# Optimization experiments

Measured on AMD Instinct MI355X. Metric: run time of the kernel, lower is better.

Reference implementation:

```python
import jax, jax.numpy as jnp
import numpy as np

N = 50000
DEG = 16
E = N * DEG
IN_F, HID, OUT_F = 512, 128, 64
SLOPE = 0.2


def setup_inputs() -> dict:
    key = jax.random.key(0)
    ks = jax.random.split(key, 10)
    row_ptr = jnp.arange(N + 1, dtype=jnp.int64) * DEG          # uniform-degree CSR
    col_idx = jax.random.randint(ks[0], (E,), 0, N, dtype=jnp.int64)
    x = jax.random.normal(ks[1], (N, IN_F), dtype=jnp.float32)
    s1 = 1.0 / np.sqrt(IN_F)
    s2 = 1.0 / np.sqrt(HID)
    return {
        "row_ptr": row_ptr,
        "col_idx": col_idx,
        "input_feature": x,
        "W1": jax.random.normal(ks[2], (IN_F, HID), dtype=jnp.float32) * s1,
        "attn_l1": jax.random.normal(ks[3], (HID,), dtype=jnp.float32) * s2,
        "attn_r1": jax.random.normal(ks[4], (HID,), dtype=jnp.float32) * s2,
        "bias1": jnp.zeros((HID,), dtype=jnp.float32),
        "W2": jax.random.normal(ks[5], (HID, OUT_F), dtype=jnp.float32) * s2,
        "attn_l2": jax.random.normal(ks[6], (OUT_F,), dtype=jnp.float32) * 0.125,
        "attn_r2": jax.random.normal(ks[7], (OUT_F,), dtype=jnp.float32) * 0.125,
        "bias2": jnp.zeros((OUT_F,), dtype=jnp.float32),
    }


def gat_layer(row_ptr, col_idx, x, W, attn_l, attn_r, bias):
    n = row_ptr.shape[0] - 1
    e = col_idx.shape[0]
    h = x @ W                                   # [N, F] dense GEMM
    el = h @ attn_l                             # [N] dst attention term
    er = h @ attn_r                             # [N] src attention term
    # edge -> destination row via CSR row_ptr
    dst = jnp.searchsorted(row_ptr, jnp.arange(e, dtype=row_ptr.dtype), side="right") - 1
    src = col_idx
    score = jax.nn.leaky_relu(el[dst] + er[src], negative_slope=SLOPE)  # [E]
    # neighborhood softmax over edges sharing a destination
    smax = jax.ops.segment_max(score, dst, num_segments=n)
    ex = jnp.exp(score - smax[dst])
    ssum = jax.ops.segment_sum(ex, dst, num_segments=n)
    alpha = ex / ssum[dst]                      # [E]
    # weighted gather-scatter aggregation
    out = jax.ops.segment_sum(alpha[:, None] * h[src], dst, num_segments=n)
    return out + bias


def reference(row_ptr, col_idx, input_feature, W1, attn_l1, attn_r1, bias1,
              W2, attn_l2, attn_r2, bias2):
    x = gat_layer(row_ptr, col_idx, input_feature, W1, attn_l1, attn_r1, bias1)
    x = gat_layer(row_ptr, col_idx, x, W2, attn_l2, attn_r2, bias2)
    return x
```

## Files before the change

### kernel.cpp

```cpp
#include <hip/hip_runtime.h>
#include <hip/hip_bf16.h>

#define Nn 50000
#define DEG 16
#define IN_F 512
#define HID 128
#define OUT_F 64
#define SLOPE 0.2f

typedef __attribute__((ext_vector_type(8))) short bf16x8;
typedef __attribute__((ext_vector_type(4))) float f32x4;
typedef __attribute__((ext_vector_type(2))) float f32x2;
typedef __attribute__((ext_vector_type(4))) unsigned int u32x4;

__device__ __forceinline__ unsigned short f2bf(float f) {
    return __builtin_bit_cast(unsigned short, __float2bfloat16(f));
}
__device__ __forceinline__ float bf2f(unsigned short u) {
    return __bfloat162float(__builtin_bit_cast(__hip_bfloat16, u));
}
__device__ __forceinline__ void async_copy16(const void* g, void* l) {
    __builtin_amdgcn_global_load_lds(
        (const __attribute__((address_space(1))) unsigned int*)g,
        (__attribute__((address_space(3))) unsigned int*)l, 16, 0, 0);
}

__global__ void __launch_bounds__(256) prep_kernel(
        const float* __restrict__ W1, const float* __restrict__ W2,
        const int* __restrict__ row_ptr,
        unsigned short* __restrict__ w1c, unsigned short* __restrict__ w2t,
        int* __restrict__ flag64) {
    int g = blockIdx.x * 256 + threadIdx.x;
    if (g == 0) {
        *flag64 = (row_ptr[1] == DEG) ? 0 : 1;
    }
    if (g < IN_F * HID) {
        int k = g >> 7, c = g & 127;
        int ch = k >> 7, kl = k & 127;
        int s  = kl >> 3, j = kl & 7;
        int sp = s ^ (c & 7);
        w1c[ch * 16384 + c * 128 + sp * 8 + j] = f2bf(W1[g]);
    } else {
        int g2 = g - IN_F * HID;
        if (g2 < HID * OUT_F) {
            int k = g2 >> 6, c = g2 & 63;
            w2t[c * HID + k] = f2bf(W2[g2]);
        }
    }
}

template<int K>
__global__ void __launch_bounds__(256) gemm1_lds(
        const float* __restrict__ Af, const unsigned short* __restrict__ w1c,
        const float* __restrict__ alv, const float* __restrict__ arv,
        unsigned short* __restrict__ Hb, float* __restrict__ el,
        float* __restrict__ er, int M) {
    constexpr int F   = 128;
    constexpr int NT  = 8;
    constexpr int NCH = K / 128;
    __shared__ unsigned short bt[128 * 128];

    const int tid  = threadIdx.x;
    const int lane = tid & 63;
    const int w    = tid >> 6;
    const int ln   = lane & 15, q = lane >> 4;
    const int mb   = blockIdx.x * 64 + w * 16;

    int m0 = mb + ln; if (m0 > M - 1) m0 = M - 1;
    const float* a0p = Af + (size_t)m0 * K;

    f32x4 acc[NT] = {};

    for (int ch = 0; ch < NCH; ++ch) {
        const char* gch = (const char*)w1c + ch * 32768;
        #pragma unroll
        for (int i = 0; i < 8; ++i) {
            int slot = w * 8 + i;
            async_copy16(gch + slot * 1024 + lane * 16, (char*)bt + slot * 1024);
        }
        __syncthreads();

        f32x4 ap[4][2];
        #pragma unroll
        for (int ks = 0; ks < 4; ++ks) {
            const int kk = ch * 128 + ks * 32 + q * 8;
            ap[ks][0] = *(const f32x4*)(a0p + kk);
            ap[ks][1] = *(const f32x4*)(a0p + kk + 4);
        }
        #pragma unroll
        for (int ks = 0; ks < 4; ++ks) {
            bf16x8 af;
            #pragma unroll
            for (int jj = 0; jj < 4; ++jj) {
                af[jj]     = (short)f2bf(ap[ks][0][jj]);
                af[jj + 4] = (short)f2bf(ap[ks][1][jj]);
            }
            #pragma unroll
            for (int nt = 0; nt < NT; ++nt) {
                const int c  = nt * 16 + ln;
                const int sp = (ks * 4 + q) ^ (ln & 7);
                bf16x8 bfr = *(const bf16x8*)&bt[c * 128 + sp * 8];
                acc[nt] = __builtin_amdgcn_mfma_f32_16x16x32_bf16(af, bfr, acc[nt], 0, 0, 0);
            }
        }
        __syncthreads();
    }

    float av[NT], bv[NT];
    #pragma unroll
    for (int nt = 0; nt < NT; ++nt) {
        av[nt] = alv[nt * 16 + ln];
        bv[nt] = arv[nt * 16 + ln];
    }
    #pragma unroll
    for (int r = 0; r < 4; ++r) {
        float sl = 0.f, sr = 0.f;
        #pragma unroll
        for (int nt = 0; nt < NT; ++nt) {
            float v = acc[nt][r];
            sl += v * av[nt];
            sr += v * bv[nt];
        }
        #pragma unroll
        for (int m = 1; m < 16; m <<= 1) {
            sl += __shfl_xor(sl, m);
            sr += __shfl_xor(sr, m);
        }
        int grow = mb + q * 4 + r;
        if (grow < M) {
            #pragma unroll
            for (int nt = 0; nt < NT; ++nt)
                Hb[(size_t)grow * F + nt * 16 + ln] = f2bf(acc[nt][r]);
            if (ln == 0) { el[grow] = sl; er[grow] = sr; }
        }
    }
}

__global__ void __launch_bounds__(256) fused_agg_gemm2(
        const int* __restrict__ col, const int* __restrict__ flag64,
        const float* __restrict__ el1, const float* __restrict__ er1,
        const unsigned short* __restrict__ Hb, const float* __restrict__ b1,
        const unsigned short* __restrict__ w2t,
        const float* __restrict__ al2, const float* __restrict__ ar2,
        unsigned short* __restrict__ H2, float* __restrict__ el2,
        float* __restrict__ er2) {
    constexpr int STR = 136;
    __shared__ unsigned short at[16 * STR];
    __shared__ float redl[16][4];
    __shared__ float redr[16][4];

    const int tid  = threadIdx.x;
    const int lane = tid & 63;
    const int w    = tid >> 6;
    const int ln   = lane & 15, q = lane >> 4;
    const int nb   = blockIdx.x * 16;
    const int use64 = *flag64;

    {
        int node = nb + w * 4 + q;
        int e    = node * DEG + ln;
        int src  = use64 ? (int)((const long long*)col)[e] : col[e];
        float sc = el1[node] + er1[src];
        sc = sc >= 0.f ? sc : SLOPE * sc;
        float mx = sc;
        #pragma unroll
        for (int m = 1; m < 16; m <<= 1) mx = fmaxf(mx, __shfl_xor(mx, m, 16));
        float ex = __expf(sc - mx);
        float sm = ex;
        #pragma unroll
        for (int m = 1; m < 16; m <<= 1) sm += __shfl_xor(sm, m, 16);
        float alpha = ex / sm;

        float a[8] = {};
        #pragma unroll
        for (int jj = 0; jj < DEG; ++jj) {
            int   sl_ = q * 16 + jj;
            int   sj = __shfl(src, sl_);
            float aj = __shfl(alpha, sl_);
            bf16x8 hv = *(const bf16x8*)&Hb[(size_t)sj * HID + ln * 8];
            #pragma unroll
            for (int c = 0; c < 8; ++c)
                a[c] += aj * bf2f((unsigned short)hv[c]);
        }
        unsigned int pk[4];
        #pragma unroll
        for (int c = 0; c < 4; ++c) {
            float lo = a[2 * c]     + b1[ln * 8 + 2 * c];
            float hi = a[2 * c + 1] + b1[ln * 8 + 2 * c + 1];
            pk[c] = (unsigned int)f2bf(lo) | ((unsigned int)f2bf(hi) << 16);
        }
        *(u32x4*)&at[(w * 4 + q) * STR + ln * 8] = *(u32x4*)pk;
    }
    __syncthreads();

    f32x4 acc = {};
    const unsigned short* bb = w2t + (size_t)(w * 16 + ln) * HID;
    #pragma unroll
    for (int ks = 0; ks < HID / 32; ++ks) {
        bf16x8 af  = *(const bf16x8*)&at[ln * STR + ks * 32 + q * 8];
        bf16x8 bfr = *(const bf16x8*)&bb[ks * 32 + q * 8];
        acc = __builtin_amdgcn_mfma_f32_16x16x32_bf16(af, bfr, acc, 0, 0, 0);
    }

    float av = al2[w * 16 + ln], bv = ar2[w * 16 + ln];
    #pragma unroll
    for (int r = 0; r < 4; ++r) {
        float v  = acc[r];
        float sl = v * av, sr = v * bv;
        #pragma unroll
        for (int m = 1; m < 16; m <<= 1) {
            sl += __shfl_xor(sl, m, 16);
            sr += __shfl_xor(sr, m, 16);
        }
        int rowl = q * 4 + r;
        H2[(size_t)(nb + rowl) * OUT_F + w * 16 + ln] = f2bf(v);
        if (ln == 0) { redl[rowl][w] = sl; redr[rowl][w] = sr; }
    }
    __syncthreads();
    if (tid < 16) {
        el2[nb + tid] = redl[tid][0] + redl[tid][1] + redl[tid][2] + redl[tid][3];
        er2[nb + tid] = redr[tid][0] + redr[tid][1] + redr[tid][2] + redr[tid][3];
    }
}

__global__ void __launch_bounds__(256) agg2_k(
        const int* __restrict__ col, const int* __restrict__ flag64,
        const float* __restrict__ el, const float* __restrict__ er,
        const unsigned short* __restrict__ Hb, const float* __restrict__ bias,
        float* __restrict__ out) {
    int lane = threadIdx.x & 63;
    int node = blockIdx.x * 4 + (threadIdx.x >> 6);
    int j    = lane & 15;
    int e    = node * DEG + j;
    int src  = (*flag64) ? (int)((const long long*)col)[e] : col[e];
    float sc = el[node] + er[src];
    sc = sc >= 0.f ? sc : SLOPE * sc;
    float mx = sc;
    #pragma unroll
    for (int m = 1; m < 16; m <<= 1) mx = fmaxf(mx, __shfl_xor(mx, m, 16));
    float ex = __expf(sc - mx);
    float sm = ex;
    #pragma unroll
    for (int m = 1; m < 16; m <<= 1) sm += __shfl_xor(sm, m, 16);
    float alpha = ex / sm;

    int h = lane >> 5;
    int c = lane & 31;
    float a0 = 0.f, a1 = 0.f;
    #pragma unroll
    for (int jj = 0; jj < DEG; jj += 2) {
        int   sj = __shfl(src, jj + h, 16);
        float aj = __shfl(alpha, jj + h, 16);
        unsigned int hv = *(const unsigned int*)&Hb[(size_t)sj * OUT_F + c * 2];
        a0 += aj * bf2f((unsigned short)(hv & 0xffffu));
        a1 += aj * bf2f((unsigned short)(hv >> 16));
    }
    a0 += __shfl_xor(a0, 32);
    a1 += __shfl_xor(a1, 32);
    if (h == 0) {
        f32x2 o;
        o[0] = a0 + bias[c * 2];
        o[1] = a1 + bias[c * 2 + 1];
        *(f32x2*)&out[(size_t)node * OUT_F + c * 2] = o;
    }
}

extern "C" void kernel_launch(void* const* d_in, const int* in_sizes, int n_in,
                              void* d_out, int out_size, void* d_ws, size_t ws_size,
                              hipStream_t stream) {
    const int*   row_ptr = (const int*)d_in[0];
    const int*   col_idx = (const int*)d_in[1];
    const float* x   = (const float*)d_in[2];
    const float* W1  = (const float*)d_in[3];
    const float* al1 = (const float*)d_in[4];
    const float* ar1 = (const float*)d_in[5];
    const float* b1  = (const float*)d_in[6];
    const float* W2  = (const float*)d_in[7];
    const float* al2 = (const float*)d_in[8];
    const float* ar2 = (const float*)d_in[9];
    const float* b2  = (const float*)d_in[10];
    float* out = (float*)d_out;

    float* ws = (float*)d_ws;
    unsigned short* h1b = (unsigned short*)ws;
    unsigned short* h2b = (unsigned short*)(ws + 3200000);
    float* el1 = ws + 5000000;
    float* er1 = ws + 5050000;
    float* el2 = ws + 5100000;
    float* er2 = ws + 5150000;
    unsigned short* w1c = (unsigned short*)(ws + 5200000);
    unsigned short* w2t = (unsigned short*)(ws + 5232768);
    int* flag64 = (int*)(ws + 5236864);

    prep_kernel<<<(IN_F * HID + HID * OUT_F + 255) / 256, 256, 0, stream>>>(
        W1, W2, row_ptr, w1c, w2t, flag64);

    gemm1_lds<512><<<(Nn + 63) / 64, 256, 0, stream>>>(
        x, w1c, al1, ar1, h1b, el1, er1, Nn);

    fused_agg_gemm2<<<Nn / 16, 256, 0, stream>>>(
        col_idx, flag64, el1, er1, h1b, b1, w2t, al2, ar2, h2b, el2, er2);

    agg2_k<<<Nn / 4, 256, 0, stream>>>(col_idx, flag64, el2, er2, h2b, b2, out);
}
```

Before: 231.9 us.

## Fold W1·W2 into one 512x64 weight and aggregate projected features

Because aggregation is linear, layer-1 aggregation followed by the W2 projection is reordered. The code precomputes W12 = W1·W2, the attention vectors W1·attn_l1 and W1·attn_r1, and bias1·W2 in a prep kernel. The main GEMM now produces a 64-wide G = x·W12 directly, with el1/er1 computed as dot products of x against the folded vectors, and it drops the LDS staging of the weights. Layer-1 aggregation then gathers 64-wide bf16 rows instead of 128-wide ones, and the fused GEMM2 stage disappears. The cost is different rounding from the bf16 folded weights, plus uncached direct global loads of the weights inside the GEMM.

```diff
diff --git a/kernel.cpp b/kernel.cpp
--- a/kernel.cpp
+++ b/kernel.cpp
@@ -10,7 +10,6 @@
 
 typedef __attribute__((ext_vector_type(8))) short bf16x8;
 typedef __attribute__((ext_vector_type(4))) float f32x4;
-typedef __attribute__((ext_vector_type(2))) float f32x2;
 typedef __attribute__((ext_vector_type(4))) unsigned int u32x4;
 
 __device__ __forceinline__ unsigned short f2bf(float f) {
@@ -19,47 +18,51 @@
 __device__ __forceinline__ float bf2f(unsigned short u) {
     return __bfloat162float(__builtin_bit_cast(__hip_bfloat16, u));
 }
-__device__ __forceinline__ void async_copy16(const void* g, void* l) {
-    __builtin_amdgcn_global_load_lds(
-        (const __attribute__((address_space(1))) unsigned int*)g,
-        (__attribute__((address_space(3))) unsigned int*)l, 16, 0, 0);
-}
 
 __global__ void __launch_bounds__(256) prep_kernel(
         const float* __restrict__ W1, const float* __restrict__ W2,
-        const int* __restrict__ row_ptr,
-        unsigned short* __restrict__ w1c, unsigned short* __restrict__ w2t,
-        int* __restrict__ flag64) {
-    int g = blockIdx.x * 256 + threadIdx.x;
-    if (g == 0) {
+        const float* __restrict__ al1, const float* __restrict__ ar1,
+        const float* __restrict__ b1, const int* __restrict__ row_ptr,
+        unsigned short* __restrict__ w12t, float* __restrict__ uv,
+        float* __restrict__ c2v, int* __restrict__ flag64) {
+    const int tid = threadIdx.x;
+    const int lane = tid & 63;
+    const int w = tid >> 6;
+    const int k = blockIdx.x * 4 + w;
+    if (blockIdx.x == 0 && tid == 0) {
         *flag64 = (row_ptr[1] == DEG) ? 0 : 1;
     }
-    if (g < IN_F * HID) {
-        int k = g >> 7, c = g & 127;
-        int ch = k >> 7, kl = k & 127;
-        int s  = kl >> 3, j = kl & 7;
-        int sp = s ^ (c & 7);
-        w1c[ch * 16384 + c * 128 + sp * 8 + j] = f2bf(W1[g]);
-    } else {
-        int g2 = g - IN_F * HID;
-        if (g2 < HID * OUT_F) {
-            int k = g2 >> 6, c = g2 & 63;
-            w2t[c * HID + k] = f2bf(W2[g2]);
-        }
+    const float* w1row = W1 + (size_t)k * HID;
+
+    float acc = 0.f;
+    #pragma unroll 8
+    for (int j = 0; j < HID; ++j)
+        acc += w1row[j] * W2[j * OUT_F + lane];
+    w12t[(size_t)lane * IN_F + k] = f2bf(acc);
+
+    float pu = w1row[lane] * al1[lane] + w1row[lane + 64] * al1[lane + 64];
+    float pv = w1row[lane] * ar1[lane] + w1row[lane + 64] * ar1[lane + 64];
+    #pragma unroll
+    for (int m = 1; m < 64; m <<= 1) {
+        pu += __shfl_xor(pu, m);
+        pv += __shfl_xor(pv, m);
+    }
+    if (lane == 0) { uv[k] = pu; uv[IN_F + k] = pv; }
+
+    if (blockIdx.x == 0 && w == 0) {
+        float cacc = 0.f;
+        #pragma unroll 8
+        for (int j = 0; j < HID; ++j) cacc += b1[j] * W2[j * OUT_F + lane];
+        c2v[lane] = cacc;
     }
 }
 
 template<int K>
-__global__ void __launch_bounds__(256) gemm1_lds(
-        const float* __restrict__ Af, const unsigned short* __restrict__ w1c,
-        const float* __restrict__ alv, const float* __restrict__ arv,
-        unsigned short* __restrict__ Hb, float* __restrict__ el,
+__global__ void __launch_bounds__(256) gemm1_direct(
+        const float* __restrict__ Af, const unsigned short* __restrict__ w12t,
+        const float* __restrict__ uv,
+        unsigned short* __restrict__ G, float* __restrict__ el,
         float* __restrict__ er, int M) {
-    constexpr int F   = 128;
-    constexpr int NT  = 8;
-    constexpr int NCH = K / 128;
-    __shared__ unsigned short bt[128 * 128];
-
     const int tid  = threadIdx.x;
     const int lane = tid & 63;
     const int w    = tid >> 6;
@@ -69,170 +72,65 @@
     int m0 = mb + ln; if (m0 > M - 1) m0 = M - 1;
     const float* a0p = Af + (size_t)m0 * K;
 
-    f32x4 acc[NT] = {};
-
-    for (int ch = 0; ch < NCH; ++ch) {
-        const char* gch = (const char*)w1c + ch * 32768;
-        #pragma unroll
-        for (int i = 0; i < 8; ++i) {
-            int slot = w * 8 + i;
-            async_copy16(gch + slot * 1024 + lane * 16, (char*)bt + slot * 1024);
-        }
-        __syncthreads();
-
-        f32x4 ap[4][2];
-        #pragma unroll
-        for (int ks = 0; ks < 4; ++ks) {
-            const int kk = ch * 128 + ks * 32 + q * 8;
-            ap[ks][0] = *(const f32x4*)(a0p + kk);
-            ap[ks][1] = *(const f32x4*)(a0p + kk + 4);
-        }
-        #pragma unroll
-        for (int ks = 0; ks < 4; ++ks) {
-            bf16x8 af;
-            #pragma unroll
-            for (int jj = 0; jj < 4; ++jj) {
-                af[jj]     = (short)f2bf(ap[ks][0][jj]);
-                af[jj + 4] = (short)f2bf(ap[ks][1][jj]);
-            }
-            #pragma unroll
-            for (int nt = 0; nt < NT; ++nt) {
-                const int c  = nt * 16 + ln;
-                const int sp = (ks * 4 + q) ^ (ln & 7);
-                bf16x8 bfr = *(const bf16x8*)&bt[c * 128 + sp * 8];
-                acc[nt] = __builtin_amdgcn_mfma_f32_16x16x32_bf16(af, bfr, acc[nt], 0, 0, 0);
-            }
-        }
-        __syncthreads();
-    }
-
-    float av[NT], bv[NT];
-    #pragma unroll
-    for (int nt = 0; nt < NT; ++nt) {
-        av[nt] = alv[nt * 16 + ln];
-        bv[nt] = arv[nt * 16 + ln];
-    }
+    f32x4 acc[4] = {};
+    float sl = 0.f, sr = 0.f;
+
+    #pragma unroll 4
+    for (int ks = 0; ks < K / 32; ++ks) {
+        const int kk = ks * 32 + q * 8;
+        f32x4 ap0 = *(const f32x4*)(a0p + kk);
+        f32x4 ap1 = *(const f32x4*)(a0p + kk + 4);
+        f32x4 u0  = *(const f32x4*)(uv + kk);
+        f32x4 u1_ = *(const f32x4*)(uv + kk + 4);
+        f32x4 v0  = *(const f32x4*)(uv + K + kk);
+        f32x4 v1_ = *(const f32x4*)(uv + K + kk + 4);
+        bf16x8 af;
+        #pragma unroll
+        for (int jj = 0; jj < 4; ++jj) {
+            af[jj]     = (short)f2bf(ap0[jj]);
+            af[jj + 4] = (short)f2bf(ap1[jj]);
+            sl += ap0[jj] * u0[jj] + ap1[jj] * u1_[jj];
+            sr += ap0[jj] * v0[jj] + ap1[jj] * v1_[jj];
+        }
+        #pragma unroll
+        for (int nt = 0; nt < 4; ++nt) {
+            bf16x8 bfr = *(const bf16x8*)&w12t[(size_t)(nt * 16 + ln) * K + kk];
+            acc[nt] = __builtin_amdgcn_mfma_f32_16x16x32_bf16(af, bfr, acc[nt], 0, 0, 0);
+        }
+    }
+
+    sl += __shfl_xor(sl, 16); sl += __shfl_xor(sl, 32);
+    sr += __shfl_xor(sr, 16); sr += __shfl_xor(sr, 32);
+    if (q == 0 && mb + ln < M) { el[mb + ln] = sl; er[mb + ln] = sr; }
+
     #pragma unroll
     for (int r = 0; r < 4; ++r) {
-        float sl = 0.f, sr = 0.f;
-        #pragma unroll
-        for (int nt = 0; nt < NT; ++nt) {
-            float v = acc[nt][r];
-            sl += v * av[nt];
-            sr += v * bv[nt];
-        }
-        #pragma unroll
-        for (int m = 1; m < 16; m <<= 1) {
-            sl += __shfl_xor(sl, m);
-            sr += __shfl_xor(sr, m);
-        }
         int grow = mb + q * 4 + r;
         if (grow < M) {
             #pragma unroll
-            for (int nt = 0; nt < NT; ++nt)
-                Hb[(size_t)grow * F + nt * 16 + ln] = f2bf(acc[nt][r]);
-            if (ln == 0) { el[grow] = sl; er[grow] = sr; }
-        }
-    }
-}
-
-__global__ void __launch_bounds__(256) fused_agg_gemm2(
+            for (int nt = 0; nt < 4; ++nt)
+                G[(size_t)grow * OUT_F + nt * 16 + ln] = f2bf(acc[nt][r]);
+        }
+    }
+}
+
+template<int MODE>
+__global__ void __launch_bounds__(256) agg_k(
         const int* __restrict__ col, const int* __restrict__ flag64,
-        const float* __restrict__ el1, const float* __restrict__ er1,
-        const unsigned short* __restrict__ Hb, const float* __restrict__ b1,
-        const unsigned short* __restrict__ w2t,
-        const float* __restrict__ al2, const float* __restrict__ ar2,
-        unsigned short* __restrict__ H2, float* __restrict__ el2,
-        float* __restrict__ er2) {
-    constexpr int STR = 136;
-    __shared__ unsigned short at[16 * STR];
-    __shared__ float redl[16][4];
-    __shared__ float redr[16][4];
-
+        const float* __restrict__ el, const float* __restrict__ er,
+        const unsigned short* __restrict__ Hs, const float* __restrict__ addv,
+        const float* __restrict__ alv, const float* __restrict__ arv,
+        unsigned short* __restrict__ Ho, float* __restrict__ elo,
+        float* __restrict__ ero, float* __restrict__ Fo) {
     const int tid  = threadIdx.x;
     const int lane = tid & 63;
     const int w    = tid >> 6;
     const int ln   = lane & 15, q = lane >> 4;
-    const int nb   = blockIdx.x * 16;
+    const int node = blockIdx.x * 16 + w * 4 + q;
     const int use64 = *flag64;
 
-    {
-        int node = nb + w * 4 + q;
-        int e    = node * DEG + ln;
-        int src  = use64 ? (int)((const long long*)col)[e] : col[e];
-        float sc = el1[node] + er1[src];
-        sc = sc >= 0.f ? sc : SLOPE * sc;
-        float mx = sc;
-        #pragma unroll
-        for (int m = 1; m < 16; m <<= 1) mx = fmaxf(mx, __shfl_xor(mx, m, 16));
-        float ex = __expf(sc - mx);
-        float sm = ex;
-        #pragma unroll
-        for (int m = 1; m < 16; m <<= 1) sm += __shfl_xor(sm, m, 16);
-        float alpha = ex / sm;
-
-        float a[8] = {};
-        #pragma unroll
-        for (int jj = 0; jj < DEG; ++jj) {
-            int   sl_ = q * 16 + jj;
-            int   sj = __shfl(src, sl_);
-            float aj = __shfl(alpha, sl_);
-            bf16x8 hv = *(const bf16x8*)&Hb[(size_t)sj * HID + ln * 8];
-            #pragma unroll
-            for (int c = 0; c < 8; ++c)
-                a[c] += aj * bf2f((unsigned short)hv[c]);
-        }
-        unsigned int pk[4];
-        #pragma unroll
-        for (int c = 0; c < 4; ++c) {
-            float lo = a[2 * c]     + b1[ln * 8 + 2 * c];
-            float hi = a[2 * c + 1] + b1[ln * 8 + 2 * c + 1];
-            pk[c] = (unsigned int)f2bf(lo) | ((unsigned int)f2bf(hi) << 16);
-        }
-        *(u32x4*)&at[(w * 4 + q) * STR + ln * 8] = *(u32x4*)pk;
-    }
-    __syncthreads();
-
-    f32x4 acc = {};
-    const unsigned short* bb = w2t + (size_t)(w * 16 + ln) * HID;
-    #pragma unroll
-    for (int ks = 0; ks < HID / 32; ++ks) {
-        bf16x8 af  = *(const bf16x8*)&at[ln * STR + ks * 32 + q * 8];
-        bf16x8 bfr = *(const bf16x8*)&bb[ks * 32 + q * 8];
-        acc = __builtin_amdgcn_mfma_f32_16x16x32_bf16(af, bfr, acc, 0, 0, 0);
-    }
-
-    float av = al2[w * 16 + ln], bv = ar2[w * 16 + ln];
-    #pragma unroll
-    for (int r = 0; r < 4; ++r) {
-        float v  = acc[r];
-        float sl = v * av, sr = v * bv;
-        #pragma unroll
-        for (int m = 1; m < 16; m <<= 1) {
-            sl += __shfl_xor(sl, m, 16);
-            sr += __shfl_xor(sr, m, 16);
-        }
-        int rowl = q * 4 + r;
-        H2[(size_t)(nb + rowl) * OUT_F + w * 16 + ln] = f2bf(v);
-        if (ln == 0) { redl[rowl][w] = sl; redr[rowl][w] = sr; }
-    }
-    __syncthreads();
-    if (tid < 16) {
-        el2[nb + tid] = redl[tid][0] + redl[tid][1] + redl[tid][2] + redl[tid][3];
-        er2[nb + tid] = redr[tid][0] + redr[tid][1] + redr[tid][2] + redr[tid][3];
-    }
-}
-
-__global__ void __launch_bounds__(256) agg2_k(
-        const int* __restrict__ col, const int* __restrict__ flag64,
-        const float* __restrict__ el, const float* __restrict__ er,
-        const unsigned short* __restrict__ Hb, const float* __restrict__ bias,
-        float* __restrict__ out) {
-    int lane = threadIdx.x & 63;
-    int node = blockIdx.x * 4 + (threadIdx.x >> 6);
-    int j    = lane & 15;
-    int e    = node * DEG + j;
-    int src  = (*flag64) ? (int)((const long long*)col)[e] : col[e];
+    int e   = node * DEG + ln;
+    int src = use64 ? (int)((const long long*)col)[e] : col[e];
     float sc = el[node] + er[src];
     sc = sc >= 0.f ? sc : SLOPE * sc;
     float mx = sc;
@@ -244,24 +142,52 @@
     for (int m = 1; m < 16; m <<= 1) sm += __shfl_xor(sm, m, 16);
     float alpha = ex / sm;
 
-    int h = lane >> 5;
-    int c = lane & 31;
-    float a0 = 0.f, a1 = 0.f;
+    const int half = ln >> 3, cc = ln & 7;
+    float a[8] = {};
     #pragma unroll
     for (int jj = 0; jj < DEG; jj += 2) {
-        int   sj = __shfl(src, jj + h, 16);
-        float aj = __shfl(alpha, jj + h, 16);
-        unsigned int hv = *(const unsigned int*)&Hb[(size_t)sj * OUT_F + c * 2];
-        a0 += aj * bf2f((unsigned short)(hv & 0xffffu));
-        a1 += aj * bf2f((unsigned short)(hv >> 16));
-    }
-    a0 += __shfl_xor(a0, 32);
-    a1 += __shfl_xor(a1, 32);
-    if (h == 0) {
-        f32x2 o;
-        o[0] = a0 + bias[c * 2];
-        o[1] = a1 + bias[c * 2 + 1];
-        *(f32x2*)&out[(size_t)node * OUT_F + c * 2] = o;
+        int   sj = __shfl(src, jj + half, 16);
+        float aj = __shfl(alpha, jj + half, 16);
+        bf16x8 hv = *(const bf16x8*)&Hs[(size_t)sj * OUT_F + cc * 8];
+        #pragma unroll
+        for (int c = 0; c < 8; ++c)
+            a[c] += aj * bf2f((unsigned short)hv[c]);
+    }
+    #pragma unroll
+    for (int c = 0; c < 8; ++c) {
+        a[c] += __shfl_xor(a[c], 8, 16);
+        a[c] += addv[cc * 8 + c];
+    }
+
+    if (MODE == 0) {
+        float pl = 0.f, pr = 0.f;
+        #pragma unroll
+        for (int c = 0; c < 8; ++c) {
+            pl += a[c] * alv[cc * 8 + c];
+            pr += a[c] * arv[cc * 8 + c];
+        }
+        #pragma unroll
+        for (int m = 1; m < 8; m <<= 1) {
+            pl += __shfl_xor(pl, m, 16);
+            pr += __shfl_xor(pr, m, 16);
+        }
+        if (ln == 0) { elo[node] = pl; ero[node] = pr; }
+        if (half == 0) {
+            unsigned int pk[4];
+            #pragma unroll
+            for (int c = 0; c < 4; ++c)
+                pk[c] = (unsigned int)f2bf(a[2 * c]) |
+                        ((unsigned int)f2bf(a[2 * c + 1]) << 16);
+            *(u32x4*)&Ho[(size_t)node * OUT_F + cc * 8] = *(u32x4*)pk;
+        }
+    } else {
+        if (half == 0) {
+            f32x4 o0, o1;
+            #pragma unroll
+            for (int c = 0; c < 4; ++c) { o0[c] = a[c]; o1[c] = a[c + 4]; }
+            *(f32x4*)&Fo[(size_t)node * OUT_F + cc * 8]     = o0;
+            *(f32x4*)&Fo[(size_t)node * OUT_F + cc * 8 + 4] = o1;
+        }
     }
 }
 
@@ -282,24 +208,27 @@
     float* out = (float*)d_out;
 
     float* ws = (float*)d_ws;
-    unsigned short* h1b = (unsigned short*)ws;
-    unsigned short* h2b = (unsigned short*)(ws + 3200000);
-    float* el1 = ws + 5000000;
-    float* er1 = ws + 5050000;
-    float* el2 = ws + 5100000;
-    float* er2 = ws + 5150000;
-    unsigned short* w1c = (unsigned short*)(ws + 5200000);
-    unsigned short* w2t = (unsigned short*)(ws + 5232768);
-    int* flag64 = (int*)(ws + 5236864);
-
-    prep_kernel<<<(IN_F * HID + HID * OUT_F + 255) / 256, 256, 0, stream>>>(
-        W1, W2, row_ptr, w1c, w2t, flag64);
-
-    gemm1_lds<512><<<(Nn + 63) / 64, 256, 0, stream>>>(
-        x, w1c, al1, ar1, h1b, el1, er1, Nn);
-
-    fused_agg_gemm2<<<Nn / 16, 256, 0, stream>>>(
-        col_idx, flag64, el1, er1, h1b, b1, w2t, al2, ar2, h2b, el2, er2);
-
-    agg2_k<<<Nn / 4, 256, 0, stream>>>(col_idx, flag64, el2, er2, h2b, b2, out);
-}
+    unsigned short* g   = (unsigned short*)ws;
+    unsigned short* h2b = (unsigned short*)(ws + 1600000);
+    float* el1 = ws + 3200000;
+    float* er1 = ws + 3250000;
+    float* el2 = ws + 3300000;
+    float* er2 = ws + 3350000;
+    unsigned short* w12t = (unsigned short*)(ws + 3400000);
+    float* uv  = ws + 3420000;
+    float* c2v = ws + 3421024;
+    int* flag64 = (int*)(ws + 3421100);
+
+    prep_kernel<<<128, 256, 0, stream>>>(
+        W1, W2, al1, ar1, b1, row_ptr, w12t, uv, c2v, flag64);
+
+    gemm1_direct<IN_F><<<(Nn + 63) / 64, 256, 0, stream>>>(
+        x, w12t, uv, g, el1, er1, Nn);
+
+    agg_k<0><<<Nn / 16, 256, 0, stream>>>(
+        col_idx, flag64, el1, er1, g, c2v, al2, ar2, h2b, el2, er2, nullptr);
+
+    agg_k<1><<<Nn / 16, 256, 0, stream>>>(
+        col_idx, flag64, el2, er2, h2b, b2, nullptr, nullptr,
+        nullptr, nullptr, nullptr, out);
+}
```

Result: slower. 241.9 us (+4.3%).
